# Kernel tuning notes

Hardware: AMD Instinct MI355X
Metric: run time of the kernel (lower is better)

## Reference

```python
import jax, jax.numpy as jnp
import numpy as np

N_NODES, N_EDGES = 50000, 400000
F_IN, H, L, C = 8, 64, 3, 1
E_IN = 2 * H + 1 + 1  # feats_i, feats_j, edge_attr(1), rel_dist(1)


def setup_inputs() -> dict:
    key = jax.random.key(0)
    ks = jax.random.split(key, 16)
    s = 0.05
    return {
        "x": jax.random.normal(ks[0], (N_NODES, F_IN), jnp.float32),
        "pos": jax.random.normal(ks[1], (N_NODES, 3), jnp.float32),
        "edge_index": jax.random.randint(ks[2], (2, N_EDGES), 0, N_NODES),
        "edge_attr": jax.random.normal(ks[3], (N_EDGES, 1), jnp.float32),
        "embedW": jax.random.normal(ks[4], (F_IN, H), jnp.float32) * s,
        "embedb": jnp.zeros((H,), jnp.float32),
        "eW1": jax.random.normal(ks[5], (L, E_IN, 2 * E_IN), jnp.float32) * s,
        "eb1": jnp.zeros((L, 2 * E_IN), jnp.float32),
        "eW2": jax.random.normal(ks[6], (L, 2 * E_IN, H), jnp.float32) * s,
        "eb2": jnp.zeros((L, H), jnp.float32),
        "cW1": jax.random.normal(ks[7], (L, H, 4 * H), jnp.float32) * s,
        "cb1": jnp.zeros((L, 4 * H), jnp.float32),
        "cW2": jax.random.normal(ks[8], (L, 4 * H, 1), jnp.float32) * s,
        "cb2": jnp.zeros((L, 1), jnp.float32),
        "nW1": jax.random.normal(ks[9], (L, 2 * H, 2 * H), jnp.float32) * s,
        "nb1": jnp.zeros((L, 2 * H), jnp.float32),
        "nW2": jax.random.normal(ks[10], (L, 2 * H, H), jnp.float32) * s,
        "nb2": jnp.zeros((L, H), jnp.float32),
        "linW": jax.random.normal(ks[11], (H, C), jnp.float32) * s,
        "linb": jnp.zeros((C,), jnp.float32),
    }


def reference(x, pos, edge_index, edge_attr, embedW, embedb,
              eW1, eb1, eW2, eb2, cW1, cb1, cW2, cb2,
              nW1, nb1, nW2, nb2, linW, linb):
    silu = jax.nn.silu
    row, col = edge_index[0], edge_index[1]  # target i, source j
    feats = x @ embedW + embedb              # [N, H] initial node embedding
    coors = pos                              # [N, 3]
    for l in range(L):  # fixed small layer loop
        rel = coors[row] - coors[col]                            # [E, 3]
        dist = jnp.sum(rel * rel, axis=-1, keepdims=True)        # [E, 1]
        e_in = jnp.concatenate([feats[row], feats[col], edge_attr, dist], axis=-1)
        # edge_mlp: Linear -> SiLU -> Linear -> SiLU
        m = silu(silu(e_in @ eW1[l] + eb1[l]) @ eW2[l] + eb2[l])  # [E, H]
        # coors_mlp: Linear -> SiLU -> Linear -> scalar weight per edge
        cw = silu(m @ cW1[l] + cb1[l]) @ cW2[l] + cb2[l]          # [E, 1]
        coors = coors + jax.ops.segment_sum(cw * rel, row, num_segments=N_NODES)
        m_i = jax.ops.segment_sum(m, row, num_segments=N_NODES)  # [N, H]
        h = jnp.concatenate([feats, m_i], axis=-1)                # [N, 2H]
        # node_mlp: Linear -> SiLU -> Linear, residual on feats
        feats = feats + (silu(h @ nW1[l] + nb1[l]) @ nW2[l] + nb2[l])
    return feats @ linW + linb  # [N, C]
```

## Files before the change

kernel.cpp:

```cpp
#include <hip/hip_runtime.h>
#include <hip/hip_bf16.h>

#define NN 50000
#define NNP 50048
#define NE 400000
#define FH 64
#define NTILES (NE / 64)
#define CHUNK 782

typedef __attribute__((ext_vector_type(8))) short short8;
typedef __attribute__((ext_vector_type(8))) _Float16 half8;
typedef __attribute__((ext_vector_type(4))) float float4v;

__device__ __forceinline__ float silu_f(float x) {
    return x * __builtin_amdgcn_rcpf(1.0f + __expf(-x));
}
__device__ __forceinline__ short f2h(float f) {
    _Float16 h = (_Float16)f;
    return *(short*)&h;
}
__device__ __forceinline__ float h2f(short s) {
    _Float16 h = *(_Float16*)&s;
    return (float)h;
}

__device__ __forceinline__ void frag_body(const float* __restrict__ src,
                                          short* __restrict__ dst,
                                          int t, int K, int N, int KT, int dup,
                                          int perL, int srcL) {
    int l = t / perL, tt = t - l * perL;
    int j = tt & 7, lane = (tt >> 3) & 63, frag = tt >> 9;
    int nt = frag / KT, kt = frag - nt * KT;
    int k = kt * 32 + ((lane >> 4) << 3) + j;
    int n = nt * 16 + (lane & 15);
    if (k == dup) k = dup - 1;
    float v = (k < K && n < N) ? src[(size_t)l * srcL + k * N + n] : 0.f;
    dst[t] = f2h(v);
}

__global__ void prep_all(const float* __restrict__ eW1, const float* __restrict__ eW2,
                         const float* __restrict__ cW1, const float* __restrict__ nW1,
                         const float* __restrict__ nW2, const float* __restrict__ eb1,
                         short* W1f, short* W2f, short* cW1f, short* nW1f,
                         short* nW2f, float* b1p, int* __restrict__ deg) {
    int t = blockIdx.x * 256 + threadIdx.x;
    if (t < 130560) { frag_body(eW1, W1f, t, 131, 260, 5, 130, 43520, 33800); return; }
    t -= 130560;
    if (t < 55296) { frag_body(eW2, W2f, t, 260, 64, 9, -1, 18432, 16640); return; }
    t -= 55296;
    if (t < 49152) { frag_body(cW1, cW1f, t, 64, 256, 2, -1, 16384, 16384); return; }
    t -= 49152;
    if (t < 49152) { frag_body(nW1, nW1f, t, 128, 128, 4, -1, 16384, 16384); return; }
    t -= 49152;
    if (t < 24576) { frag_body(nW2, nW2f, t, 128, 64, 4, -1, 8192, 8192); return; }
    t -= 24576;
    if (t < 816) { int l = t / 272, c = t - l * 272; b1p[t] = (c < 260) ? eb1[l * 260 + c] : 0.f; return; }
    t -= 816;
    if (t < NN + 1) deg[t] = 0;
}

__global__ void embed_kernel(const float* __restrict__ x, const float* __restrict__ W,
                             const float* __restrict__ b, const float* __restrict__ pos,
                             float* __restrict__ feats, short* __restrict__ featsh,
                             float* __restrict__ cA) {
    int t = blockIdx.x * 256 + threadIdx.x;
    if (t >= NN * FH) return;
    int n = t >> 6, hcol = t & 63;
    float acc = b[hcol];
    #pragma unroll
    for (int k = 0; k < 8; k++) acc += x[n * 8 + k] * W[k * FH + hcol];
    feats[t] = acc;
    featsh[t] = f2h(acc);
    if (hcol < 3) cA[n * 3 + hcol] = pos[n * 3 + hcol];
}

__global__ void hist_kernel(const int* __restrict__ ei, int* __restrict__ deg) {
    int e = blockIdx.x * 256 + threadIdx.x;
    if (e >= NE) return;
    atomicAdd(&deg[ei[e]], 1);
}

__global__ void alloc_kernel(const int* __restrict__ deg, int* __restrict__ off,
                             int* __restrict__ cursor, int* __restrict__ gcount) {
    __shared__ int s[256];
    __shared__ int base;
    int t = threadIdx.x, n = blockIdx.x * 256 + t;
    int d = (n < NN) ? deg[n] : 0;
    s[t] = d;
    __syncthreads();
    for (int st = 1; st < 256; st <<= 1) {
        int v = (t >= st) ? s[t - st] : 0;
        __syncthreads();
        s[t] += v;
        __syncthreads();
    }
    if (t == 255) base = atomicAdd(gcount, s[255]);
    __syncthreads();
    if (n < NN) { int o = base + s[t] - d; off[n] = o; cursor[n] = o; }
}

__global__ void fill_kernel(const int* __restrict__ ei, const float* __restrict__ eattr,
                            int* __restrict__ cursor, int* __restrict__ erow,
                            int* __restrict__ ecol, float* __restrict__ eattrp) {
    int e = blockIdx.x * 256 + threadIdx.x;
    if (e >= NE) return;
    int r = ei[e];
    int p = atomicAdd(&cursor[r], 1);
    erow[p] = r;
    ecol[p] = ei[NE + e];
    eattrp[p] = eattr[e];
}

#define SE_STRIDE 168
#define H1_STRIDE 296
#define M_STRIDE  72

__global__ __launch_bounds__(256, 3) void edge_fused(
    const int* __restrict__ erow, const int* __restrict__ ecol,
    const float* __restrict__ eattrp,
    const short* __restrict__ featsh, const float* __restrict__ coors,
    const short* __restrict__ W1f, const float* __restrict__ b1p,
    const short* __restrict__ W2f, const float* __restrict__ b2,
    const short* __restrict__ cW1f, const float* __restrict__ cb1,
    const float* __restrict__ cW2, const float* __restrict__ cb2,
    short* __restrict__ m_edge, float* __restrict__ cwrel)
{
    __shared__ char smem[48896];
    short* sE   = (short*)smem;
    short* sH1  = (short*)smem;
    short* sM   = (short*)(smem + 37888);
    float* sRel = (float*)(smem + 47104);
    float* cwbuf = (float*)(smem + 47872);

    int b = blockIdx.x;
    int kb = (b & 7) * CHUNK + (b >> 3);
    if (kb >= NTILES) return;
    int k0 = kb * 64;

    int t = threadIdx.x;
    int lane = t & 63, wid = t >> 6, quad = lane >> 4, lc = lane & 15;

    {
        int el = t >> 2, sub = t & 3, k = k0 + el;
        int rI = erow[k], cI = ecol[k];
        const short8* fr = (const short8*)(featsh + (size_t)rI * FH);
        const short8* fc = (const short8*)(featsh + (size_t)cI * FH);
        short* er = sE + el * SE_STRIDE;
        *(short8*)(er + sub * 16) = fr[sub * 2];
        *(short8*)(er + sub * 16 + 8) = fr[sub * 2 + 1];
        *(short8*)(er + 64 + sub * 16) = fc[sub * 2];
        *(short8*)(er + 64 + sub * 16 + 8) = fc[sub * 2 + 1];
        #pragma unroll
        for (int i = 0; i < 10; i++) er[128 + sub * 10 + i] = 0;
        if (sub == 0) {
            float rx = coors[rI * 3 + 0] - coors[cI * 3 + 0];
            float ry = coors[rI * 3 + 1] - coors[cI * 3 + 1];
            float rz = coors[rI * 3 + 2] - coors[cI * 3 + 2];
            float dist = rx * rx + ry * ry + rz * rz;
            short dh = f2h(dist);
            er[128] = f2h(eattrp[k]);
            er[129] = dh;
            er[130] = f2h(dist - h2f(dh));
            sRel[el * 3 + 0] = rx; sRel[el * 3 + 1] = ry; sRel[el * 3 + 2] = rz;
        }
    }
    __syncthreads();

    half8 af[4][5];
    #pragma unroll
    for (int m = 0; m < 4; m++)
        #pragma unroll
        for (int kt = 0; kt < 5; kt++)
            af[m][kt] = *(const half8*)(sE + (m * 16 + lc) * SE_STRIDE + kt * 32 + quad * 8);
    __syncthreads();

    {
        *(long long*)(sH1 + (t >> 2) * H1_STRIDE + 272 + (t & 3) * 4) = 0LL;
        #pragma unroll
        for (int i = 0; i < 4; i++) {
            int nt = wid + i * 4;
            float bias = b1p[nt * 16 + lc];
            float4v acc[4];
            #pragma unroll
            for (int m = 0; m < 4; m++) acc[m] = (float4v){bias, bias, bias, bias};
            #pragma unroll
            for (int kt = 0; kt < 5; kt++) {
                half8 bh = ((const half8*)(W1f + (size_t)(nt * 5 + kt) * 512))[lane];
                #pragma unroll
                for (int m = 0; m < 4; m++)
                    acc[m] = __builtin_amdgcn_mfma_f32_16x16x32_f16(af[m][kt], bh, acc[m], 0, 0, 0);
            }
            #pragma unroll
            for (int m = 0; m < 4; m++)
                #pragma unroll
                for (int r = 0; r < 4; r++)
                    sH1[(m * 16 + quad * 4 + r) * H1_STRIDE + nt * 16 + lc] = f2h(silu_f(acc[m][r]));
        }
        if (wid == 0) {
            const int nt = 16;
            float bias = b1p[nt * 16 + lc];
            float4v acc[4];
            #pragma unroll
            for (int m = 0; m < 4; m++) acc[m] = (float4v){bias, bias, bias, bias};
            #pragma unroll
            for (int kt = 0; kt < 5; kt++) {
                half8 bh = ((const half8*)(W1f + (size_t)(nt * 5 + kt) * 512))[lane];
                #pragma unroll
                for (int m = 0; m < 4; m++)
                    acc[m] = __builtin_amdgcn_mfma_f32_16x16x32_f16(af[m][kt], bh, acc[m], 0, 0, 0);
            }
            #pragma unroll
            for (int m = 0; m < 4; m++)
                #pragma unroll
                for (int r = 0; r < 4; r++)
                    sH1[(m * 16 + quad * 4 + r) * H1_STRIDE + nt * 16 + lc] = f2h(silu_f(acc[m][r]));
        }
    }
    __syncthreads();

    {
        int nt = wid;
        float bias = b2[nt * 16 + lc];
        float4v acc[4];
        #pragma unroll
        for (int m = 0; m < 4; m++) acc[m] = (float4v){bias, bias, bias, bias};
        #pragma unroll
        for (int kt = 0; kt < 9; kt++) {
            half8 bh = ((const half8*)(W2f + (size_t)(nt * 9 + kt) * 512))[lane];
            #pragma unroll
            for (int m = 0; m < 4; m++) {
                half8 a = *(const half8*)(sH1 + (m * 16 + lc) * H1_STRIDE + kt * 32 + quad * 8);
                acc[m] = __builtin_amdgcn_mfma_f32_16x16x32_f16(a, bh, acc[m], 0, 0, 0);
            }
        }
        #pragma unroll
        for (int m = 0; m < 4; m++)
            #pragma unroll
            for (int r = 0; r < 4; r++)
                sM[(m * 16 + quad * 4 + r) * M_STRIDE + nt * 16 + lc] = f2h(silu_f(acc[m][r]));
    }
    __syncthreads();

    {
        int row = t >> 2, c0 = (t & 3) * 16;
        short8 v0 = *(const short8*)(sM + row * M_STRIDE + c0);
        short8 v1 = *(const short8*)(sM + row * M_STRIDE + c0 + 8);
        short* mg = m_edge + (size_t)(k0 + row) * FH + c0;
        *(short8*)(mg) = v0;
        *(short8*)(mg + 8) = v1;
    }
    {
        half8 ag[4][2];
        #pragma unroll
        for (int m = 0; m < 4; m++)
            #pragma unroll
            for (int kt = 0; kt < 2; kt++)
                ag[m][kt] = *(const half8*)(sM + (m * 16 + lc) * M_STRIDE + kt * 32 + quad * 8);
        float cwpart[4][4];
        #pragma unroll
        for (int m = 0; m < 4; m++)
            #pragma unroll
            for (int r = 0; r < 4; r++) cwpart[m][r] = 0.f;
        #pragma unroll
        for (int i = 0; i < 4; i++) {
            int nt = wid + i * 4;
            float bias = cb1[nt * 16 + lc];
            float4v acc[4];
            #pragma unroll
            for (int m = 0; m < 4; m++) acc[m] = (float4v){bias, bias, bias, bias};
            #pragma unroll
            for (int kt = 0; kt < 2; kt++) {
                half8 bh = ((const half8*)(cW1f + (size_t)(nt * 2 + kt) * 512))[lane];
                #pragma unroll
                for (int m = 0; m < 4; m++)
                    acc[m] = __builtin_amdgcn_mfma_f32_16x16x32_f16(ag[m][kt], bh, acc[m], 0, 0, 0);
            }
            float wv = cW2[nt * 16 + lc];
            #pragma unroll
            for (int m = 0; m < 4; m++)
                #pragma unroll
                for (int r = 0; r < 4; r++)
                    cwpart[m][r] += silu_f(acc[m][r]) * wv;
        }
        #pragma unroll
        for (int m = 0; m < 4; m++)
            #pragma unroll
            for (int r = 0; r < 4; r++) {
                float p = cwpart[m][r];
                p += __shfl_xor(p, 1);
                p += __shfl_xor(p, 2);
                p += __shfl_xor(p, 4);
                p += __shfl_xor(p, 8);
                if (lc == 0) cwbuf[wid * 64 + m * 16 + quad * 4 + r] = p;
            }
    }
    __syncthreads();

    if (t < 64) {
        float cw = cb2[0] + cwbuf[t] + cwbuf[64 + t] + cwbuf[128 + t] + cwbuf[192 + t];
        float* o = cwrel + (size_t)(k0 + t) * 3;
        o[0] = cw * sRel[t * 3 + 0];
        o[1] = cw * sRel[t * 3 + 1];
        o[2] = cw * sRel[t * 3 + 2];
    }
}

#define HS 136
__global__ __launch_bounds__(256, 4) void agg_node(
    const int* __restrict__ off, const int* __restrict__ deg,
    const short* __restrict__ m_edge, const float* __restrict__ cwrel,
    const float* __restrict__ coors_in, float* __restrict__ coors_out,
    float* __restrict__ feats, short* __restrict__ featsh,
    const short* __restrict__ W1f, const float* __restrict__ b1,
    const short* __restrict__ W2f, const float* __restrict__ b2)
{
    __shared__ short sh[64 * HS];
    __shared__ short sg[64 * HS];
    int t = threadIdx.x, lane = t & 63, wid = t >> 6, quad = lane >> 4, lc = lane & 15;
    int n0 = blockIdx.x * 64;

    {
        int row = t >> 2, sub = t & 3;
        const short8* fp = (const short8*)(featsh + (size_t)(n0 + row) * FH);
        *(short8*)(sh + row * HS + sub * 16) = fp[sub * 2];
        *(short8*)(sh + row * HS + sub * 16 + 8) = fp[sub * 2 + 1];
    }
    for (int nn = 0; nn < 16; nn++) {
        int row = wid * 16 + nn;
        int n = n0 + row;
        float sum = 0.f, cv = 0.f;
        if (n < NN) {
            int s = off[n], e = s + deg[n];
            float s0 = 0.f, s1 = 0.f, s2 = 0.f, s3 = 0.f;
            int k = s;
            for (; k + 3 < e; k += 4) {
                s0 += h2f(m_edge[(size_t)k * FH + lane]);
                s1 += h2f(m_edge[(size_t)(k + 1) * FH + lane]);
                s2 += h2f(m_edge[(size_t)(k + 2) * FH + lane]);
                s3 += h2f(m_edge[(size_t)(k + 3) * FH + lane]);
                if (lane < 3)
                    cv += (cwrel[(size_t)k * 3 + lane] + cwrel[(size_t)(k + 1) * 3 + lane])
                        + (cwrel[(size_t)(k + 2) * 3 + lane] + cwrel[(size_t)(k + 3) * 3 + lane]);
            }
            for (; k < e; k++) {
                s0 += h2f(m_edge[(size_t)k * FH + lane]);
                if (lane < 3) cv += cwrel[(size_t)k * 3 + lane];
            }
            sum = (s0 + s1) + (s2 + s3);
            if (lane < 3) coors_out[n * 3 + lane] = coors_in[n * 3 + lane] + cv;
        }
        sh[row * HS + 64 + lane] = f2h(sum);
    }
    __syncthreads();

    half8 af[4][4];
    #pragma unroll
    for (int m = 0; m < 4; m++)
        #pragma unroll
        for (int kt = 0; kt < 4; kt++)
            af[m][kt] = *(const half8*)(sh + (m * 16 + lc) * HS + kt * 32 + quad * 8);
    #pragma unroll
    for (int i = 0; i < 2; i++) {
        int nt = wid + i * 4;
        float bias = b1[nt * 16 + lc];
        float4v acc[4];
        #pragma unroll
        for (int m = 0; m < 4; m++) acc[m] = (float4v){bias, bias, bias, bias};
        #pragma unroll
        for (int kt = 0; kt < 4; kt++) {
            half8 bh = ((const half8*)(W1f + (size_t)(nt * 4 + kt) * 512))[lane];
            #pragma unroll
            for (int m = 0; m < 4; m++)
                acc[m] = __builtin_amdgcn_mfma_f32_16x16x32_f16(af[m][kt], bh, acc[m], 0, 0, 0);
        }
        #pragma unroll
        for (int m = 0; m < 4; m++)
            #pragma unroll
            for (int r = 0; r < 4; r++)
                sg[(m * 16 + quad * 4 + r) * HS + nt * 16 + lc] = f2h(silu_f(acc[m][r]));
    }
    __syncthreads();

    {
        int nt = wid;
        float bias = b2[nt * 16 + lc];
        float4v acc[4];
        #pragma unroll
        for (int m = 0; m < 4; m++) acc[m] = (float4v){bias, bias, bias, bias};
        #pragma unroll
        for (int kt = 0; kt < 4; kt++) {
            half8 bh = ((const half8*)(W2f + (size_t)(nt * 4 + kt) * 512))[lane];
            #pragma unroll
            for (int m = 0; m < 4; m++) {
                half8 a = *(const half8*)(sg + (m * 16 + lc) * HS + kt * 32 + quad * 8);
                acc[m] = __builtin_amdgcn_mfma_f32_16x16x32_f16(a, bh, acc[m], 0, 0, 0);
            }
        }
        #pragma unroll
        for (int m = 0; m < 4; m++)
            #pragma unroll
            for (int r = 0; r < 4; r++) {
                int row = m * 16 + quad * 4 + r;
                size_t idx = (size_t)(n0 + row) * FH + nt * 16 + lc;
                float nv = feats[idx] + acc[m][r];
                feats[idx] = nv;
                featsh[idx] = f2h(nv);
            }
    }
}

__global__ void final_kernel(const float* __restrict__ feats, const float* __restrict__ linW,
                             const float* __restrict__ linb, float* __restrict__ out) {
    int t = blockIdx.x * 256 + threadIdx.x;
    int n = t >> 6;
    int lane = threadIdx.x & 63;
    if (n >= NN) return;
    float v = feats[(size_t)n * FH + lane] * linW[lane];
    #pragma unroll
    for (int off = 32; off > 0; off >>= 1) v += __shfl_down(v, off);
    if (lane == 0) out[n] = v + linb[0];
}

extern "C" void kernel_launch(void* const* d_in, const int* in_sizes, int n_in,
                              void* d_out, int out_size, void* d_ws, size_t ws_size,
                              hipStream_t stream) {
    const float* x      = (const float*)d_in[0];
    const float* pos    = (const float*)d_in[1];
    const int*   ei     = (const int*)d_in[2];
    const float* eattr  = (const float*)d_in[3];
    const float* embedW = (const float*)d_in[4];
    const float* embedb = (const float*)d_in[5];
    const float* eW1    = (const float*)d_in[6];
    const float* eb1    = (const float*)d_in[7];
    const float* eW2    = (const float*)d_in[8];
    const float* eb2    = (const float*)d_in[9];
    const float* cW1    = (const float*)d_in[10];
    const float* cb1    = (const float*)d_in[11];
    const float* cW2    = (const float*)d_in[12];
    const float* cb2    = (const float*)d_in[13];
    const float* nW1    = (const float*)d_in[14];
    const float* nb1    = (const float*)d_in[15];
    const float* nW2    = (const float*)d_in[16];
    const float* nb2    = (const float*)d_in[17];
    const float* linW   = (const float*)d_in[18];
    const float* linb   = (const float*)d_in[19];
    float* out = (float*)d_out;

    char* wp = (char*)d_ws;
    auto alloc = [&](size_t bytes) { void* p = wp; wp += (bytes + 255) & ~(size_t)255; return p; };

    const int W1F_L  = 17 * 5 * 512;
    const int W2F_L  = 4 * 9 * 512;
    const int CW1F_L = 16 * 2 * 512;
    const int NW1F_L = 8 * 4 * 512;
    const int NW2F_L = 4 * 4 * 512;

    float* feats  = (float*)alloc((size_t)NNP * FH * 4);
    short* featsh = (short*)alloc((size_t)NNP * FH * 2);
    float* cA     = (float*)alloc((size_t)NN * 3 * 4);
    float* cB     = (float*)alloc((size_t)NN * 3 * 4);
    short* W1f    = (short*)alloc((size_t)3 * W1F_L * 2);
    short* W2f    = (short*)alloc((size_t)3 * W2F_L * 2);
    short* cW1f   = (short*)alloc((size_t)3 * CW1F_L * 2);
    short* nW1f   = (short*)alloc((size_t)3 * NW1F_L * 2);
    short* nW2f   = (short*)alloc((size_t)3 * NW2F_L * 2);
    float* b1p    = (float*)alloc((size_t)3 * 272 * 4);
    int*   deg    = (int*)alloc((size_t)(NN + 1) * 4);
    int*   off    = (int*)alloc((size_t)NN * 4);
    int*   cursor = (int*)alloc((size_t)NN * 4);
    int*   erow   = (int*)alloc((size_t)NE * 4);
    int*   ecol   = (int*)alloc((size_t)NE * 4);
    float* eattrp = (float*)alloc((size_t)NE * 4);
    short* m_edge = (short*)alloc((size_t)NE * FH * 2);
    float* cwrel  = (float*)alloc((size_t)NE * 3 * 4);
    int* gcount = deg + NN;

    prep_all<<<(359553 + 255) / 256, 256, 0, stream>>>(
        eW1, eW2, cW1, nW1, nW2, eb1,
        W1f, W2f, cW1f, nW1f, nW2f, b1p, deg);

    hist_kernel<<<(NE + 255) / 256, 256, 0, stream>>>(ei, deg);
    alloc_kernel<<<(NN + 255) / 256, 256, 0, stream>>>(deg, off, cursor, gcount);
    fill_kernel<<<(NE + 255) / 256, 256, 0, stream>>>(ei, eattr, cursor, erow, ecol, eattrp);

    embed_kernel<<<(NN * FH + 255) / 256, 256, 0, stream>>>(x, embedW, embedb, pos, feats, featsh, cA);

    float* ccur = cA;
    float* cnext = cB;
    for (int l = 0; l < 3; l++) {
        edge_fused<<<8 * CHUNK, 256, 0, stream>>>(
            erow, ecol, eattrp, featsh, ccur,
            W1f + (size_t)l * W1F_L, b1p + l * 272,
            W2f + (size_t)l * W2F_L, eb2 + l * 64,
            cW1f + (size_t)l * CW1F_L, cb1 + l * 256,
            cW2 + l * 256, cb2 + l,
            m_edge, cwrel);
        agg_node<<<NNP / 64, 256, 0, stream>>>(
            off, deg, m_edge, cwrel, ccur, cnext, feats, featsh,
            nW1f + (size_t)l * NW1F_L, nb1 + l * 128,
            nW2f + (size_t)l * NW2F_L, nb2 + l * 64);
        float* tmp = ccur; ccur = cnext; cnext = tmp;
    }
    final_kernel<<<(NN * FH) / 256, 256, 0, stream>>>(feats, linW, linb, out);
}
```

Baseline: 639.3 us.

## Skip dead coordinate MLP in last layer and fuse final linear into aggregation

In the last layer the coordinate update is never used by the output, so the edge kernel skips the coors MLP (a 64x256 matmul per edge plus the cwrel write) and the node kernel skips the cwrel gather and the coors write. The final linear projection is folded into the last agg_node launch using a shuffle and shared-memory reduction, which removes the final_kernel launch and the last feats/featsh writeback. The cost is extra branching, plus a __syncthreads placed inside a uniform conditional.

Result: faster. 582.2 us (-8.9%).

```diff
diff --git a/kernel.cpp b/kernel.cpp
--- a/kernel.cpp
+++ b/kernel.cpp
@@ -123,7 +123,7 @@
     const short* __restrict__ W2f, const float* __restrict__ b2,
     const short* __restrict__ cW1f, const float* __restrict__ cb1,
     const float* __restrict__ cW2, const float* __restrict__ cb2,
-    short* __restrict__ m_edge, float* __restrict__ cwrel)
+    short* __restrict__ m_edge, float* __restrict__ cwrel, int do_cw)
 {
     __shared__ char smem[48896];
     short* sE   = (short*)smem;
@@ -249,7 +249,7 @@
         *(short8*)(mg) = v0;
         *(short8*)(mg + 8) = v1;
     }
-    {
+    if (do_cw) {
         half8 ag[4][2];
         #pragma unroll
         for (int m = 0; m < 4; m++)
@@ -293,15 +293,15 @@
                 p += __shfl_xor(p, 8);
                 if (lc == 0) cwbuf[wid * 64 + m * 16 + quad * 4 + r] = p;
             }
-    }
-    __syncthreads();
-
-    if (t < 64) {
-        float cw = cb2[0] + cwbuf[t] + cwbuf[64 + t] + cwbuf[128 + t] + cwbuf[192 + t];
-        float* o = cwrel + (size_t)(k0 + t) * 3;
-        o[0] = cw * sRel[t * 3 + 0];
-        o[1] = cw * sRel[t * 3 + 1];
-        o[2] = cw * sRel[t * 3 + 2];
+        __syncthreads();
+
+        if (t < 64) {
+            float cw = cb2[0] + cwbuf[t] + cwbuf[64 + t] + cwbuf[128 + t] + cwbuf[192 + t];
+            float* o = cwrel + (size_t)(k0 + t) * 3;
+            o[0] = cw * sRel[t * 3 + 0];
+            o[1] = cw * sRel[t * 3 + 1];
+            o[2] = cw * sRel[t * 3 + 2];
+        }
     }
 }
 
@@ -312,7 +312,9 @@
     const float* __restrict__ coors_in, float* __restrict__ coors_out,
     float* __restrict__ feats, short* __restrict__ featsh,
     const short* __restrict__ W1f, const float* __restrict__ b1,
-    const short* __restrict__ W2f, const float* __restrict__ b2)
+    const short* __restrict__ W2f, const float* __restrict__ b2,
+    const float* __restrict__ linW, const float* __restrict__ linb,
+    float* __restrict__ out, int last)
 {
     __shared__ short sh[64 * HS];
     __shared__ short sg[64 * HS];
@@ -338,16 +340,16 @@
                 s1 += h2f(m_edge[(size_t)(k + 1) * FH + lane]);
                 s2 += h2f(m_edge[(size_t)(k + 2) * FH + lane]);
                 s3 += h2f(m_edge[(size_t)(k + 3) * FH + lane]);
-                if (lane < 3)
+                if (!last && lane < 3)
                     cv += (cwrel[(size_t)k * 3 + lane] + cwrel[(size_t)(k + 1) * 3 + lane])
                         + (cwrel[(size_t)(k + 2) * 3 + lane] + cwrel[(size_t)(k + 3) * 3 + lane]);
             }
             for (; k < e; k++) {
                 s0 += h2f(m_edge[(size_t)k * FH + lane]);
-                if (lane < 3) cv += cwrel[(size_t)k * 3 + lane];
+                if (!last && lane < 3) cv += cwrel[(size_t)k * 3 + lane];
             }
             sum = (s0 + s1) + (s2 + s3);
-            if (lane < 3) coors_out[n * 3 + lane] = coors_in[n * 3 + lane] + cv;
+            if (!last && lane < 3) coors_out[n * 3 + lane] = coors_in[n * 3 + lane] + cv;
         }
         sh[row * HS + 64 + lane] = f2h(sum);
     }
@@ -396,29 +398,50 @@
                 acc[m] = __builtin_amdgcn_mfma_f32_16x16x32_f16(a, bh, acc[m], 0, 0, 0);
             }
         }
-        #pragma unroll
-        for (int m = 0; m < 4; m++)
-            #pragma unroll
-            for (int r = 0; r < 4; r++) {
-                int row = m * 16 + quad * 4 + r;
-                size_t idx = (size_t)(n0 + row) * FH + nt * 16 + lc;
-                float nv = feats[idx] + acc[m][r];
-                feats[idx] = nv;
-                featsh[idx] = f2h(nv);
-            }
-    }
-}
-
-__global__ void final_kernel(const float* __restrict__ feats, const float* __restrict__ linW,
-                             const float* __restrict__ linb, float* __restrict__ out) {
-    int t = blockIdx.x * 256 + threadIdx.x;
-    int n = t >> 6;
-    int lane = threadIdx.x & 63;
-    if (n >= NN) return;
-    float v = feats[(size_t)n * FH + lane] * linW[lane];
-    #pragma unroll
-    for (int off = 32; off > 0; off >>= 1) v += __shfl_down(v, off);
-    if (lane == 0) out[n] = v + linb[0];
+        if (!last) {
+            #pragma unroll
+            for (int m = 0; m < 4; m++)
+                #pragma unroll
+                for (int r = 0; r < 4; r++) {
+                    int row = m * 16 + quad * 4 + r;
+                    size_t idx = (size_t)(n0 + row) * FH + nt * 16 + lc;
+                    float nv = feats[idx] + acc[m][r];
+                    feats[idx] = nv;
+                    featsh[idx] = f2h(nv);
+                }
+        } else {
+            float lw = linW[nt * 16 + lc];
+            float v[4][4];
+            #pragma unroll
+            for (int m = 0; m < 4; m++)
+                #pragma unroll
+                for (int r = 0; r < 4; r++) {
+                    int row = m * 16 + quad * 4 + r;
+                    size_t idx = (size_t)(n0 + row) * FH + nt * 16 + lc;
+                    v[m][r] = (feats[idx] + acc[m][r]) * lw;
+                }
+            __syncthreads();
+            float* red = (float*)sg;
+            #pragma unroll
+            for (int m = 0; m < 4; m++)
+                #pragma unroll
+                for (int r = 0; r < 4; r++) {
+                    float p = v[m][r];
+                    p += __shfl_xor(p, 1);
+                    p += __shfl_xor(p, 2);
+                    p += __shfl_xor(p, 4);
+                    p += __shfl_xor(p, 8);
+                    if (lc == 0) red[(m * 16 + quad * 4 + r) * 4 + wid] = p;
+                }
+            __syncthreads();
+            if (t < 64) {
+                int n = n0 + t;
+                if (n < NN)
+                    out[n] = (red[t * 4 + 0] + red[t * 4 + 1])
+                           + (red[t * 4 + 2] + red[t * 4 + 3]) + linb[0];
+            }
+        }
+    }
 }
 
 extern "C" void kernel_launch(void* const* d_in, const int* in_sizes, int n_in,
@@ -488,18 +511,19 @@
     float* ccur = cA;
     float* cnext = cB;
     for (int l = 0; l < 3; l++) {
+        int last = (l == 2);
         edge_fused<<<8 * CHUNK, 256, 0, stream>>>(
             erow, ecol, eattrp, featsh, ccur,
             W1f + (size_t)l * W1F_L, b1p + l * 272,
             W2f + (size_t)l * W2F_L, eb2 + l * 64,
             cW1f + (size_t)l * CW1F_L, cb1 + l * 256,
             cW2 + l * 256, cb2 + l,
-            m_edge, cwrel);
+            m_edge, cwrel, last ? 0 : 1);
         agg_node<<<NNP / 64, 256, 0, stream>>>(
             off, deg, m_edge, cwrel, ccur, cnext, feats, featsh,
             nW1f + (size_t)l * NW1F_L, nb1 + l * 128,
-            nW2f + (size_t)l * NW2F_L, nb2 + l * 64);
+            nW2f + (size_t)l * NW2F_L, nb2 + l * 64,
+            linW, linb, out, last);
         float* tmp = ccur; ccur = cnext; cnext = tmp;
     }
-    final_kernel<<<(NN * FH) / 256, 256, 0, stream>>>(feats, linW, linb, out);
-}
+}
```
